# Performance work log

Hardware: AMD Instinct MI355X
Metric: run time of the kernel (lower is better)

## Reference

```python
import jax, jax.numpy as jnp
import numpy as np

B, Lq, D = 2, 4096, 768
NH, NP, NL = 6, 4, 1
Hs, Ws = 128, 128
Lf = Hs * Ws
DH = D // NH
EPS = 1e-6


def _ln(x, g, b):
    m = jnp.mean(x, -1, keepdims=True)
    v = jnp.mean(jnp.square(x - m), -1, keepdims=True)
    return (x - m) * jax.lax.rsqrt(v + EPS) * g + b


def setup_inputs() -> dict:
    key = jax.random.key(0)
    ks = jax.random.split(key, 20)
    s = 0.02
    rn = lambda k, shape, sc=s: (jax.random.normal(k, shape, jnp.float32) * sc)
    return {
        'query': jax.random.normal(ks[0], (B, Lq, D), jnp.float32),
        'reference_points': jax.random.uniform(ks[1], (B, Lq, NL, 2), jnp.float32),
        'feat': jax.random.normal(ks[2], (B, Lf, D), jnp.float32),
        'feat_other_modalities': jax.random.normal(ks[3], (B, Lq, D), jnp.float32),
        'spatial_shapes': jnp.array([[Hs, Ws]], jnp.int32),
        'level_start_index': jnp.array([0], jnp.int32),
        'qn_g': jnp.ones(D), 'qn_b': jnp.zeros(D),
        'fn_g': jnp.ones(D), 'fn_b': jnp.zeros(D),
        'W_off': rn(ks[4], (D, NH * NL * NP * 2)), 'b_off': jnp.zeros(NH * NL * NP * 2),
        'W_attn': rn(ks[5], (D, NH * NL * NP)), 'b_attn': jnp.zeros(NH * NL * NP),
        'W_val': rn(ks[6], (D, D)), 'b_val': jnp.zeros(D),
        'W_out': rn(ks[7], (D, D)), 'b_out': jnp.zeros(D),
        'gamma': rn(ks[8], (D,), 0.1),
        'qnm_g': jnp.ones(D), 'qnm_b': jnp.zeros(D),
        'fnm_g': jnp.ones(D), 'fnm_b': jnp.zeros(D),
        'ada_w0': rn(ks[9], (D, D // 4)), 'ada_b0': jnp.zeros(D // 4),
        'ada_w1': rn(ks[10], (D, D // 4)), 'ada_b1': jnp.zeros(D // 4),
        'ada_w2': rn(ks[11], (D // 4, D)), 'ada_b2': jnp.zeros(D),
        'gamma_om': rn(ks[12], (D,), 0.1),
    }


def _msdeform_attn(query_n, reference_points, feat_n, Hi, Wi,
                   W_off, b_off, W_attn, b_attn, W_val, b_val, W_out, b_out):
    Bv = query_n.shape[0]
    value = (feat_n @ W_val + b_val).reshape(Bv, Lf, NH, DH)
    value = value.transpose(0, 2, 1, 3)  # (B, NH, Lf, DH)

    off = (query_n @ W_off + b_off).reshape(Bv, Lq, NH, NL, NP, 2)
    aw = (query_n @ W_attn + b_attn).reshape(Bv, Lq, NH, NL * NP)
    aw = jax.nn.softmax(aw, axis=-1).reshape(Bv, Lq, NH, NL, NP)

    normalizer = jnp.array([Wi, Hi], jnp.float32)  # [W, H]
    loc = reference_points[:, :, None, :, None, :] + off / normalizer  # (B,Lq,NH,NL,NP,2)
    loc = loc[:, :, :, 0]  # single level -> (B, Lq, NH, NP, 2)

    # grid_sample align_corners=False, padding zeros
    x = loc[..., 0] * Wi - 0.5
    y = loc[..., 1] * Hi - 0.5
    x0 = jnp.floor(x); y0 = jnp.floor(y)
    wx1 = x - x0; wx0 = 1.0 - wx1
    wy1 = y - y0; wy0 = 1.0 - wy1
    x0i = x0.astype(jnp.int32); y0i = y0.astype(jnp.int32)
    x1i = x0i + 1; y1i = y0i + 1

    def t(a):  # (B,Lq,NH,NP) -> (B,NH,Lq,NP,1)
        return a.transpose(0, 2, 1, 3)[..., None]

    def gather(yy, xx):
        valid = (xx >= 0) & (xx < Wi) & (yy >= 0) & (yy < Hi)
        idx = jnp.clip(yy, 0, Hi - 1) * Wi + jnp.clip(xx, 0, Wi - 1)  # (B,Lq,NH,NP)
        idx = idx.transpose(0, 2, 1, 3).reshape(Bv, NH, Lq * NP)
        g = jnp.take_along_axis(value, idx[..., None], axis=2)  # (B,NH,Lq*NP,DH)
        g = g.reshape(Bv, NH, Lq, NP, DH)
        return g * t(valid.astype(jnp.float32))

    sampled = (gather(y0i, x0i) * t(wy0 * wx0) + gather(y0i, x1i) * t(wy0 * wx1)
               + gather(y1i, x0i) * t(wy1 * wx0) + gather(y1i, x1i) * t(wy1 * wx1))
    awT = aw[:, :, :, 0].transpose(0, 2, 1, 3)[..., None]  # (B,NH,Lq,NP,1)
    out = jnp.sum(sampled * awT, axis=3)  # (B,NH,Lq,DH)
    out = out.transpose(0, 2, 1, 3).reshape(Bv, Lq, D)
    return out @ W_out + b_out


def reference(query, reference_points, feat, feat_other_modalities, spatial_shapes,
              level_start_index, qn_g, qn_b, fn_g, fn_b, W_off, b_off, W_attn, b_attn,
              W_val, b_val, W_out, b_out, gamma, qnm_g, qnm_b, fnm_g, fnm_b,
              ada_w0, ada_b0, ada_w1, ada_b1, ada_w2, ada_b2, gamma_om):
    Hi = int(np.asarray(spatial_shapes)[0, 0]); Wi = int(np.asarray(spatial_shapes)[0, 1])
    query_n = _ln(query, qn_g, qn_b)
    feat_n = _ln(feat, fn_g, fn_b)
    attn = _msdeform_attn(query_n, reference_points, feat_n, Hi, Wi,
                          W_off, b_off, W_attn, b_attn, W_val, b_val, W_out, b_out)
    q = query + gamma * attn
    fom_n = _ln(feat_other_modalities, fnm_g, fnm_b)
    qn2 = _ln(q, qnm_g, qnm_b)
    p = qn2 @ ada_w0 + ada_b0
    xm = fom_n @ ada_w1 + ada_b1
    prompted = (p + xm) @ ada_w2 + ada_b2
    q = q + gamma_om * prompted
    return (q, prompted)
```

## Files before the change

### kernel.cpp

```cpp
#include <hip/hip_runtime.h>
#include <hip/hip_bf16.h>

typedef long long i64;

#define B_   2
#define LQ   4096
#define D_   768
#define NH_  6
#define NP_  4
#define DH_  128
#define LF   16384
#define NQ_ROWS (B_*LQ)
#define NF_ROWS (B_*LF)
#define QSIZE (NQ_ROWS*D_)
#define LN2_BLOCKS (2*NQ_ROWS/8)

typedef __bf16 bf16x8 __attribute__((ext_vector_type(8)));
typedef float  f32x4  __attribute__((ext_vector_type(4)));

__device__ __forceinline__ int probe_bf(const void* probe) {
  return (*(const unsigned*)probe == 0x3F803F80u) ? 1 : 0;
}
__device__ __forceinline__ float load_in(const void* p, i64 i, int bf) {
  if (bf) return __bfloat162float(((const __hip_bfloat16*)p)[i]);
  return ((const float*)p)[i];
}
__device__ __forceinline__ float us2f(unsigned short u) {
  unsigned v = (unsigned)u << 16;
  return __uint_as_float(v);
}
__device__ __forceinline__ unsigned short f2us(float f) {
  __hip_bfloat16 h = __float2bfloat16(f);
  return *(unsigned short*)&h;
}

#define NCVT 17
struct CvtArgs { const void* src[NCVT]; const void* src2[NCVT]; float* dst[NCVT]; int n[NCVT]; const void* probe; };
__global__ void k_cvt(CvtArgs a) {
  int bf = probe_bf(a.probe);
  int ai = blockIdx.y;
  int n = a.n[ai];
  const void* s = a.src[ai];
  const void* s2 = a.src2[ai];
  float* d = a.dst[ai];
  for (int i = blockIdx.x * blockDim.x + threadIdx.x; i < n; i += gridDim.x * blockDim.x) {
    float v = load_in(s, i, bf);
    if (s2) v += load_in(s2, i, bf);
    d[i] = v;
  }
}

__global__ void k_colsum(const void* w, const void* g, const void* b,
                         float* c, float* d, const void* probe) {
  __shared__ float red[2][4][64];
  int bf = probe_bf(probe);
  int l = threadIdx.x & 63;
  int kc = threadIdx.x >> 6;
  int j = blockIdx.x * 64 + l;
  int k0 = kc * 192;
  float cs = 0.f, ds = 0.f;
  #pragma unroll 8
  for (int k = 0; k < 192; ++k) {
    float wv = load_in(w, (i64)(k0 + k) * 768 + j, bf);
    cs += load_in(g, k0 + k, bf) * wv;
    ds += load_in(b, k0 + k, bf) * wv;
  }
  red[0][kc][l] = cs; red[1][kc][l] = ds;
  __syncthreads();
  if (kc == 0) {
    c[j] = red[0][0][l] + red[0][1][l] + red[0][2][l] + red[0][3][l];
    d[j] = red[1][0][l] + red[1][1][l] + red[1][2][l] + red[1][3][l];
  }
}

__device__ __forceinline__ void ln_load_bf16(const void* src, i64 so, int sl, uint4* u) {
  const unsigned short* s = (const unsigned short*)src + so;
  #pragma unroll
  for (int j = 0; j < 3; ++j) u[j] = *(const uint4*)(s + (i64)(j * 32 + sl) * 8);
}
__device__ __forceinline__ void ln_load_f32(const void* src, i64 so, int sl, float4* w) {
  const float* s = (const float*)src + so;
  #pragma unroll
  for (int j = 0; j < 3; ++j) {
    w[2*j]   = *(const float4*)(s + (i64)(j * 32 + sl) * 8);
    w[2*j+1] = *(const float4*)(s + (i64)(j * 32 + sl) * 8 + 4);
  }
}
__device__ __forceinline__ void ln_unpack_bf16(const uint4* u, float* v) {
  #pragma unroll
  for (int j = 0; j < 3; ++j) {
    uint4 t = u[j];
    v[j*8+0] = us2f((unsigned short)t.x); v[j*8+1] = us2f((unsigned short)(t.x >> 16));
    v[j*8+2] = us2f((unsigned short)t.y); v[j*8+3] = us2f((unsigned short)(t.y >> 16));
    v[j*8+4] = us2f((unsigned short)t.z); v[j*8+5] = us2f((unsigned short)(t.z >> 16));
    v[j*8+6] = us2f((unsigned short)t.w); v[j*8+7] = us2f((unsigned short)(t.w >> 16));
  }
}
__device__ __forceinline__ void ln_unpack_f32(const float4* w, float* v) {
  #pragma unroll
  for (int j = 0; j < 6; ++j) {
    v[j*4+0] = w[j].x; v[j*4+1] = w[j].y; v[j*4+2] = w[j].z; v[j*4+3] = w[j].w;
  }
}
__device__ __forceinline__ void ln_finish(const float* v, const float* g, const float* b,
                                          unsigned short* dp, int sl) {
  float s1 = 0.f, s2 = 0.f;
  #pragma unroll
  for (int i = 0; i < 24; ++i) { s1 += v[i]; s2 += v[i] * v[i]; }
  #pragma unroll
  for (int o = 16; o > 0; o >>= 1) { s1 += __shfl_xor(s1, o, 64); s2 += __shfl_xor(s2, o, 64); }
  float mean = s1 * (1.f / 768.f);
  float var  = s2 * (1.f / 768.f) - mean * mean;
  float rstd = rsqrtf(var + 1e-6f);
  #pragma unroll
  for (int j = 0; j < 3; ++j) {
    int gi = (j * 32 + sl) * 8;
    float4 g0 = *(const float4*)(g + gi), g1 = *(const float4*)(g + gi + 4);
    float4 b0 = *(const float4*)(b + gi), b1 = *(const float4*)(b + gi + 4);
    uint4 o;
    o.x = (unsigned)f2us((v[j*8+0]-mean)*rstd*g0.x+b0.x) | ((unsigned)f2us((v[j*8+1]-mean)*rstd*g0.y+b0.y) << 16);
    o.y = (unsigned)f2us((v[j*8+2]-mean)*rstd*g0.z+b0.z) | ((unsigned)f2us((v[j*8+3]-mean)*rstd*g0.w+b0.w) << 16);
    o.z = (unsigned)f2us((v[j*8+4]-mean)*rstd*g1.x+b1.x) | ((unsigned)f2us((v[j*8+5]-mean)*rstd*g1.y+b1.y) << 16);
    o.w = (unsigned)f2us((v[j*8+6]-mean)*rstd*g1.z+b1.z) | ((unsigned)f2us((v[j*8+7]-mean)*rstd*g1.w+b1.w) << 16);
    *(uint4*)(dp + gi) = o;
  }
}

#define NTT 7
struct StageArgs {
  const void* tsrc[NTT]; __hip_bfloat16* tdst[NTT];
  const void* tscale[NTT];
  int K[NTT]; int N[NTT]; int Nt[NTT]; int ds[NTT];
  int tileBase[NTT]; int tilesN[NTT];
  const void* query; const void* fom;
  const float *qg, *qb, *mg, *mb;
  __hip_bfloat16 *qn, *qnf;
  void* qraw;
  const void* probe;
};
__global__ void k_stage(StageArgs a) {
  __shared__ float lds[64][65];
  int bf = probe_bf(a.probe);
  if ((int)blockIdx.x >= LN2_BLOCKS) {
    int t = blockIdx.x - LN2_BLOCKS;
    int e = 0;
    #pragma unroll
    for (int i = 1; i < NTT; ++i) if (t >= a.tileBase[i]) e = i;
    int lt = t - a.tileBase[e];
    int tn = lt % a.tilesN[e], tk = lt / a.tilesN[e];
    int K = a.K[e], N = a.N[e], Nt = a.Nt[e], ds = a.ds[e];
    int k0 = tk * 64, n0 = tn * 64;
    int tid = threadIdx.x;
    int cl = tid & 63, rw = tid >> 6;
    const void* s = a.tsrc[e];
    const void* sc = a.tscale[e];
    #pragma unroll
    for (int i = 0; i < 16; ++i) {
      int kl = rw * 16 + i;
      int n = n0 + cl;
      float v = (n < N) ? load_in(s, (i64)(k0 + kl) * N + n, bf) : 0.f;
      if (sc) v *= load_in(sc, k0 + kl, bf);
      lds[kl][cl] = v;
    }
    __syncthreads();
    __hip_bfloat16* d = a.tdst[e];
    #pragma unroll
    for (int i = 0; i < 16; ++i) {
      int nl = rw * 16 + i;
      int n = n0 + nl;
      if (n < Nt) d[(i64)n * ds + k0 + cl] = __float2bfloat16(lds[cl][nl]);
    }
    return;
  }
  int row = blockIdx.x * 8 + (threadIdx.x >> 5);
  int sl = threadIdx.x & 31;
  const void* s; const float *g, *b; unsigned short* dp; i64 so; int kind; int lr;
  if (row < NQ_ROWS) {
    kind = 1; lr = row; s = a.query; so = (i64)lr * 768;
    g = a.qg; b = a.qb; dp = (unsigned short*)a.qn + (i64)lr * 768;
  } else {
    kind = 2; lr = row - NQ_ROWS; s = a.fom; so = (i64)lr * 768;
    g = a.mg; b = a.mb; dp = (unsigned short*)a.qnf + (i64)lr * 1536 + 768;
  }
  float v[24];
  if (bf) {
    uint4 u[3];
    ln_load_bf16(s, so, sl, u);
    if (kind == 1) {
      unsigned short* qr = (unsigned short*)a.qraw + (i64)lr * 768;
      #pragma unroll
      for (int j = 0; j < 3; ++j) *(uint4*)(qr + (i64)(j * 32 + sl) * 8) = u[j];
    }
    ln_unpack_bf16(u, v);
  } else {
    float4 w[6];
    ln_load_f32(s, so, sl, w);
    if (kind == 1) {
      float* qr = (float*)a.qraw + (i64)lr * 768;
      #pragma unroll
      for (int j = 0; j < 3; ++j) {
        *(float4*)(qr + (i64)(j * 32 + sl) * 8)     = w[2*j];
        *(float4*)(qr + (i64)(j * 32 + sl) * 8 + 4) = w[2*j+1];
      }
    }
    ln_unpack_f32(w, v);
  }
  ln_finish(v, g, b, dp, sl);
}

__global__ void k_ln_q(const float* src, const float* g, const float* b, __hip_bfloat16* dst) {
  int hw = blockIdx.x * 8 + (threadIdx.x >> 5);
  int sl = threadIdx.x & 31;
  int r = hw * 2;
  float4 w0[6], w1[6];
  ln_load_f32(src, (i64)r * 768, sl, w0);
  ln_load_f32(src, (i64)(r + 1) * 768, sl, w1);
  float v[24];
  ln_unpack_f32(w0, v);
  ln_finish(v, g, b, (unsigned short*)dst + (i64)r * 1536, sl);
  ln_unpack_f32(w1, v);
  ln_finish(v, g, b, (unsigned short*)dst + (i64)(r + 1) * 1536, sl);
}

__device__ __forceinline__ void load_lds16(const void* g, void* l) {
  __builtin_amdgcn_global_load_lds((__attribute__((address_space(1))) void*)g,
                                   (__attribute__((address_space(3))) void*)l, 16, 0, 0);
}

__global__ void k_vgemm(const void* __restrict__ Araw, const __hip_bfloat16* __restrict__ Wt,
                        const float* __restrict__ bias, __hip_bfloat16* __restrict__ Cp,
                        const float* __restrict__ cv, const float* __restrict__ dv,
                        const void* probe) {
  __shared__ __align__(16) __hip_bfloat16 sm[2 * 8192];
  __shared__ float rowstat[128][2];
  __hip_bfloat16* As = sm;
  __hip_bfloat16* Bs = sm + 8192;
  const int tid  = threadIdx.x;
  const int w    = tid >> 6, lane = tid & 63;
  const int quad = lane >> 4, l15 = lane & 15;
  const int f = blockIdx.x;
  const int xcd = f & 7, s8 = f >> 3;
  const int bn = (s8 % 6) * 128;
  const int bm = (xcd + (s8 / 6) * 8) * 128;
  const int wm = (w >> 1) * 64, wn = (w & 1) * 64;
  const int bfv = probe_bf(probe);

  {
    int sl = tid & 31, hw = tid >> 5;
    #pragma unroll 2
    for (int pass = 0; pass < 16; ++pass) {
      int r = pass * 8 + hw;
      float v[24];
      if (bfv) { uint4 u[3]; ln_load_bf16(Araw, (i64)(bm + r) * 768, sl, u); ln_unpack_bf16(u, v); }
      else     { float4 wv[6]; ln_load_f32(Araw, (i64)(bm + r) * 768, sl, wv); ln_unpack_f32(wv, v); }
      float s1 = 0.f, s2 = 0.f;
      #pragma unroll
      for (int i = 0; i < 24; ++i) { s1 += v[i]; s2 += v[i] * v[i]; }
      #pragma unroll
      for (int o = 16; o > 0; o >>= 1) { s1 += __shfl_xor(s1, o, 64); s2 += __shfl_xor(s2, o, 64); }
      if (sl == 0) {
        float mean = s1 * (1.f / 768.f);
        float var  = s2 * (1.f / 768.f) - mean * mean;
        float rstd = rsqrtf(var + 1e-6f);
        rowstat[r][0] = rstd; rowstat[r][1] = -rstd * mean;
      }
    }
  }
  __syncthreads();

  int rowS[4], colS[4];
  #pragma unroll
  for (int j = 0; j < 4; ++j) {
    int p = j * 256 + tid;
    int r = p >> 3, pc = p & 7;
    rowS[j] = r; colS[j] = (pc ^ (r & 7)) * 8;
  }

  f32x4 acc[4][4];
  #pragma unroll
  for (int i = 0; i < 4; ++i)
    #pragma unroll
    for (int j = 0; j < 4; ++j) acc[i][j] = (f32x4){0.f, 0.f, 0.f, 0.f};

  const __hip_bfloat16* Ab = (const __hip_bfloat16*)Araw + (i64)bm * 768;
  const __hip_bfloat16* Bb = Wt + (i64)bn * 768;

  for (int k0 = 0; k0 < 768; k0 += 64) {
    if (bfv) {
      #pragma unroll
      for (int j = 0; j < 4; ++j)
        load_lds16(Ab + (i64)rowS[j] * 768 + k0 + colS[j], As + (j * 256 + w * 64) * 8);
    } else {
      #pragma unroll
      for (int j = 0; j < 4; ++j) {
        int p = j * 256 + tid;
        int r = p >> 3, pc = p & 7;
        const float* src = (const float*)Araw + (i64)(bm + r) * 768 + k0 + pc * 8;
        float4 x0 = *(const float4*)src;
        float4 x1 = *(const float4*)(src + 4);
        uint4 o;
        o.x = (unsigned)f2us(x0.x) | ((unsigned)f2us(x0.y) << 16);
        o.y = (unsigned)f2us(x0.z) | ((unsigned)f2us(x0.w) << 16);
        o.z = (unsigned)f2us(x1.x) | ((unsigned)f2us(x1.y) << 16);
        o.w = (unsigned)f2us(x1.z) | ((unsigned)f2us(x1.w) << 16);
        *(uint4*)(As + ((i64)r * 8 + (pc ^ (r & 7))) * 8) = o;
      }
    }
    #pragma unroll
    for (int j = 0; j < 4; ++j)
      load_lds16(Bb + (i64)rowS[j] * 768 + k0 + colS[j], Bs + (j * 256 + w * 64) * 8);
    __syncthreads();
    bf16x8 af[2][4], bg[2][4];
    #pragma unroll
    for (int s = 0; s < 2; ++s) {
      #pragma unroll
      for (int i = 0; i < 4; ++i) {
        int ra = wm + i * 16 + l15;
        af[s][i] = *(const bf16x8*)(As + (ra * 8 + ((s * 4 + quad) ^ (ra & 7))) * 8);
        int rb = wn + i * 16 + l15;
        bg[s][i] = *(const bf16x8*)(Bs + (rb * 8 + ((s * 4 + quad) ^ (rb & 7))) * 8);
      }
    }
    #pragma unroll
    for (int s = 0; s < 2; ++s)
      #pragma unroll
      for (int i = 0; i < 4; ++i)
        #pragma unroll
        for (int j = 0; j < 4; ++j)
          acc[i][j] = __builtin_amdgcn_mfma_f32_16x16x32_bf16(af[s][i], bg[s][j], acc[i][j], 0, 0, 0);
    __syncthreads();
  }

  #pragma unroll
  for (int j = 0; j < 4; ++j) {
    int col = bn + wn + j * 16 + l15;
    float cj = cv[col], dj = dv[col] + bias[col];
    #pragma unroll
    for (int i = 0; i < 4; ++i) {
      #pragma unroll
      for (int r = 0; r < 4; ++r) {
        int lr = wm + i * 16 + quad * 4 + r;
        float v = rowstat[lr][0] * acc[i][j][r] + rowstat[lr][1] * cj + dj;
        Cp[(i64)(bm + lr) * 768 + col] = __float2bfloat16(v);
      }
    }
  }
}

template<int EPI>
__global__ void k_mgemm(const __hip_bfloat16* __restrict__ A, const __hip_bfloat16* __restrict__ Wt,
                        const float* __restrict__ bias, void* __restrict__ Cp,
                        int M, int N, int K, int Nx,
                        const void* aux0, const float* __restrict__ aux1, const void* probe) {
  __shared__ __align__(16) __hip_bfloat16 sm[2 * 8192];
  __hip_bfloat16* As = sm;
  __hip_bfloat16* Bs = sm + 8192;
  const int tid  = threadIdx.x;
  const int w    = tid >> 6, lane = tid & 63;
  const int quad = lane >> 4, l15 = lane & 15;
  const int f = blockIdx.x;
  const int xcd = f & 7, s8 = f >> 3;
  const int bn = (s8 % Nx) * 128;
  const int bm = (xcd + (s8 / Nx) * 8) * 128;
  const int wm = (w >> 1) * 64, wn = (w & 1) * 64;
  const int bfv = (EPI == 2 || EPI == 3) ? probe_bf(probe) : 0;

  int rowS[4], colS[4];
  #pragma unroll
  for (int j = 0; j < 4; ++j) {
    int p = j * 256 + tid;
    int r = p >> 3, pc = p & 7;
    rowS[j] = r; colS[j] = (pc ^ (r & 7)) * 8;
  }

  f32x4 acc[4][4];
  #pragma unroll
  for (int i = 0; i < 4; ++i)
    #pragma unroll
    for (int j = 0; j < 4; ++j) acc[i][j] = (f32x4){0.f, 0.f, 0.f, 0.f};

  const __hip_bfloat16* Ab = A  + (i64)bm * K;
  const __hip_bfloat16* Bb = Wt + (i64)bn * K;

  for (int k0 = 0; k0 < K; k0 += 64) {
    #pragma unroll
    for (int j = 0; j < 4; ++j) {
      load_lds16(Ab + (i64)rowS[j] * K + k0 + colS[j], As + (j * 256 + w * 64) * 8);
      load_lds16(Bb + (i64)rowS[j] * K + k0 + colS[j], Bs + (j * 256 + w * 64) * 8);
    }
    __syncthreads();
    bf16x8 af[2][4], bg[2][4];
    #pragma unroll
    for (int s = 0; s < 2; ++s) {
      #pragma unroll
      for (int i = 0; i < 4; ++i) {
        int ra = wm + i * 16 + l15;
        af[s][i] = *(const bf16x8*)(As + (ra * 8 + ((s * 4 + quad) ^ (ra & 7))) * 8);
        int rb = wn + i * 16 + l15;
        bg[s][i] = *(const bf16x8*)(Bs + (rb * 8 + ((s * 4 + quad) ^ (rb & 7))) * 8);
      }
    }
    #pragma unroll
    for (int s = 0; s < 2; ++s)
      #pragma unroll
      for (int i = 0; i < 4; ++i)
        #pragma unroll
        for (int j = 0; j < 4; ++j)
          acc[i][j] = __builtin_amdgcn_mfma_f32_16x16x32_bf16(af[s][i], bg[s][j], acc[i][j], 0, 0, 0);
    __syncthreads();
  }

  #pragma unroll
  for (int j = 0; j < 4; ++j) {
    int col = bn + wn + j * 16 + l15;
    if (col >= N) continue;
    float bv = bias[col];
    #pragma unroll
    for (int i = 0; i < 4; ++i) {
      #pragma unroll
      for (int r = 0; r < 4; ++r) {
        int row = bm + wm + i * 16 + quad * 4 + r;
        float v = acc[i][j][r] + bv;
        i64 idx = (i64)row * N + col;
        if (EPI == 0) {
          ((__hip_bfloat16*)Cp)[idx] = __float2bfloat16(v);
        } else if (EPI == 1) {
          ((float*)Cp)[idx] = v;
        } else if (EPI == 2) {
          ((float*)Cp)[idx] = load_in(aux0, idx, bfv) + aux1[col] * v;
        } else {
          float qv = ((const float*)aux0)[idx] + aux1[col] * v;
          if (bfv) {
            ((__hip_bfloat16*)Cp)[idx]         = __float2bfloat16(qv);
            ((__hip_bfloat16*)Cp)[QSIZE + idx] = __float2bfloat16(v);
          } else {
            ((float*)Cp)[idx]         = qv;
            ((float*)Cp)[QSIZE + idx] = v;
          }
        }
      }
    }
  }
}

__global__ void k_sample(const __hip_bfloat16* __restrict__ val, const float* __restrict__ ref,
                         const float* __restrict__ oa, const int* __restrict__ ss,
                         __hip_bfloat16* __restrict__ out) {
  int gw = blockIdx.x * 4 + (threadIdx.x >> 6);
  if (gw >= NQ_ROWS) return;
  int lane = threadIdx.x & 63;
  int sg = lane >> 4, sl = lane & 15;
  int bq = gw, b = bq >> 12;
  int Hi = ss[0], Wi = ss[1];
  float Wf = (float)Wi, Hf = (float)Hi;
  float rx = ref[(i64)bq*2], ry = ref[(i64)bq*2 + 1];
  const float* orow = oa + (i64)bq * 72;
  const __hip_bfloat16* vb = val + (i64)b * LF * D_;
  int cx = sg & 1, cy = sg >> 1;
  #pragma unroll
  for (int h = 0; h < NH_; ++h) {
    const float* ap = orow + 48 + h*4;
    float a0 = ap[0], a1 = ap[1], a2 = ap[2], a3 = ap[3];
    float mx = fmaxf(fmaxf(a0, a1), fmaxf(a2, a3));
    float e0 = __expf(a0-mx), e1 = __expf(a1-mx), e2 = __expf(a2-mx), e3 = __expf(a3-mx);
    float inv = 1.0f / (e0+e1+e2+e3);
    float wts[4] = {e0*inv, e1*inv, e2*inv, e3*inv};
    const float* op = orow + h*8;
    float acc[8];
    #pragma unroll
    for (int e = 0; e < 8; ++e) acc[e] = 0.f;
    #pragma unroll
    for (int p = 0; p < NP_; ++p) {
      float x = rx*Wf + op[p*2+0] - 0.5f;
      float y = ry*Hf + op[p*2+1] - 0.5f;
      float xf = floorf(x), yf = floorf(y);
      int x0 = (int)xf, y0 = (int)yf;
      float wx1 = x - xf, wy1 = y - yf;
      int xi = x0 + cx, yi = y0 + cy;
      float wgt = wts[p] * (cx ? wx1 : 1.f - wx1) * (cy ? wy1 : 1.f - wy1);
      if (xi >= 0 && xi < Wi && yi >= 0 && yi < Hi) {
        bf16x8 g = *(const bf16x8*)(vb + (i64)(yi*Wi + xi)*D_ + h*DH_ + sl*8);
        #pragma unroll
        for (int e = 0; e < 8; ++e) acc[e] += wgt * (float)g[e];
      }
    }
    #pragma unroll
    for (int e = 0; e < 8; ++e) {
      acc[e] += __shfl_xor(acc[e], 16, 64);
      acc[e] += __shfl_xor(acc[e], 32, 64);
    }
    if (sg == 0) {
      uint4 o;
      o.x = (unsigned)f2us(acc[0]) | ((unsigned)f2us(acc[1]) << 16);
      o.y = (unsigned)f2us(acc[2]) | ((unsigned)f2us(acc[3]) << 16);
      o.z = (unsigned)f2us(acc[4]) | ((unsigned)f2us(acc[5]) << 16);
      o.w = (unsigned)f2us(acc[6]) | ((unsigned)f2us(acc[7]) << 16);
      *(uint4*)(out + (i64)bq*D_ + h*DH_ + sl*8) = o;
    }
  }
}

extern "C" void kernel_launch(void* const* d_in, const int* in_sizes, int n_in,
                              void* d_out, int out_size, void* d_ws, size_t ws_size,
                              hipStream_t stream) {
  char* base = (char*)d_ws;
  size_t o = 0;
  auto alloc = [&](size_t bytes) { size_t r = o; o += (bytes + 63) & ~(size_t)63; return r; };
  auto F = [&](size_t off) { return (float*)(base + off); };
  auto H = [&](size_t off) { return (__hip_bfloat16*)(base + off); };
  const void* probe = d_in[6];

  size_t REF   = alloc(NQ_ROWS*2*4);
  size_t QN_G  = alloc(768*4); size_t QN_B = alloc(768*4);
  size_t FN_G  = alloc(768*4); size_t FN_B = alloc(768*4);
  size_t BOA   = alloc(128*4);
  size_t BVAL  = alloc(768*4); size_t BOUT = alloc(768*4);
  size_t GAMMA = alloc(768*4);
  size_t QNM_G = alloc(768*4); size_t QNM_B = alloc(768*4);
  size_t FNM_G = alloc(768*4); size_t FNM_B = alloc(768*4);
  size_t AB01  = alloc(192*4);
  size_t AB2   = alloc(768*4); size_t GOM  = alloc(768*4);
  size_t CV    = alloc(768*4); size_t DV   = alloc(768*4);
  size_t WT_VAL = alloc((size_t)768*768*2);
  size_t WT_OUT = alloc((size_t)768*768*2);
  size_t WT_OA  = alloc((size_t)128*768*2);
  size_t WT_A01 = alloc((size_t)256*1536*2);
  size_t WT_A2  = alloc((size_t)768*192*2);
  size_t VALUE  = alloc((size_t)NF_ROWS*768*2);
  size_t QN     = alloc((size_t)NQ_ROWS*768*2);
  size_t QRAW   = alloc((size_t)QSIZE*4);
  size_t QNF    = alloc((size_t)NQ_ROWS*1536*2);
  size_t ATTNP  = alloc((size_t)NQ_ROWS*768*2);
  size_t PXM    = alloc((size_t)NQ_ROWS*192*2);
  size_t OA     = alloc((size_t)NQ_ROWS*72*4);
  size_t QBUF   = alloc((size_t)QSIZE*4);

  {
    CvtArgs ca;
    const int   idx[NCVT]  = {1,6,7,8,9,11,13,15,17,18,19,20,21,22,24,28,29};
    const size_t dof[NCVT] = {REF,QN_G,QN_B,FN_G,FN_B,BOA,BOA+48*4,BVAL,BOUT,GAMMA,
                              QNM_G,QNM_B,FNM_G,FNM_B,AB01,AB2,GOM};
    for (int i = 0; i < NCVT; ++i) {
      ca.src[i] = d_in[idx[i]]; ca.src2[i] = nullptr;
      ca.dst[i] = F(dof[i]); ca.n[i] = in_sizes[idx[i]];
    }
    ca.src2[14] = d_in[26];
    ca.probe = probe;
    k_cvt<<<dim3(8, NCVT), 256, 0, stream>>>(ca);
  }
  k_colsum<<<12, 256, 0, stream>>>(d_in[14], d_in[8], d_in[9], F(CV), F(DV), probe);

  int tb = 0;
  {
    StageArgs sa;
    const int   src[NTT]  = {14, 16, 10, 12, 23, 25, 27};
    const size_t dst[NTT] = {WT_VAL, WT_OUT, WT_OA, WT_OA + (size_t)48*768*2,
                             WT_A01, WT_A01 + (size_t)768*2, WT_A2};
    const int Kk[NTT] = {768, 768, 768, 768, 768,  768, 192};
    const int Nn[NTT] = {768, 768,  48,  24, 192,  192, 768};
    const int Nt[NTT] = {768, 768,  48,  80, 256,  256, 768};
    const int Ds[NTT] = {768, 768, 768, 768, 1536, 1536, 192};
    const void* sc[NTT] = {d_in[8], nullptr, nullptr, nullptr, nullptr, nullptr, nullptr};
    for (int i = 0; i < NTT; ++i) {
      sa.tsrc[i] = d_in[src[i]]; sa.tdst[i] = H(dst[i]); sa.tscale[i] = sc[i];
      sa.K[i] = Kk[i]; sa.N[i] = Nn[i]; sa.Nt[i] = Nt[i]; sa.ds[i] = Ds[i];
      sa.tilesN[i] = (Nt[i] + 63) / 64;
      sa.tileBase[i] = tb;
      tb += sa.tilesN[i] * (Kk[i] / 64);
    }
    sa.query = d_in[0]; sa.fom = d_in[3];
    sa.qg = F(QN_G);  sa.qb = F(QN_B);
    sa.mg = F(FNM_G); sa.mb = F(FNM_B);
    sa.qn = H(QN); sa.qnf = H(QNF);
    sa.qraw = base + QRAW;
    sa.probe = probe;
    k_stage<<<LN2_BLOCKS + tb, 256, 0, stream>>>(sa);
  }

  k_vgemm<<<256*6, 256, 0, stream>>>(d_in[2], H(WT_VAL), F(BVAL), H(VALUE),
                                     F(CV), F(DV), probe);
  k_mgemm<1><<<64*1, 256, 0, stream>>>(H(QN), H(WT_OA), F(BOA), F(OA),
                                       NQ_ROWS, 72, 768, 1, nullptr, nullptr, probe);
  k_sample<<<NQ_ROWS/4, 256, 0, stream>>>(H(VALUE), F(REF), F(OA), (const int*)d_in[4], H(ATTNP));
  k_mgemm<2><<<64*6, 256, 0, stream>>>(H(ATTNP), H(WT_OUT), F(BOUT), F(QBUF),
                                       NQ_ROWS, 768, 768, 6, base + QRAW, F(GAMMA), probe);
  k_ln_q<<<NQ_ROWS/16, 256, 0, stream>>>(F(QBUF), F(QNM_G), F(QNM_B), H(QNF));
  k_mgemm<0><<<64*2, 256, 0, stream>>>(H(QNF), H(WT_A01), F(AB01), H(PXM),
                                       NQ_ROWS, 192, 1536, 2, nullptr, nullptr, probe);
  k_mgemm<3><<<64*6, 256, 0, stream>>>(H(PXM), H(WT_A2), F(AB2), d_out,
                                       NQ_ROWS, 768, 192, 6, F(QBUF), F(GOM), probe);
}
```

Measured before the change: 565.6 us.

## Compute feature LayerNorm stats inside value GEMM loop and fold colsum into stage kernel

The value GEMM no longer runs a separate prologue pass over its 128-row A tile to compute LayerNorm mean and rstd. Instead it accumulates the sums and squared sums from the A tiles it already loads each K step, then reduces them with shuffles before the epilogue. The bf16 path now uses register loads and LDS stores instead of direct-to-LDS loads, which adds register pressure. The separate k_colsum launch is folded into k_stage as 12 extra blocks, removing one kernel launch.

```diff
diff --git a/kernel.cpp b/kernel.cpp
--- a/kernel.cpp
+++ b/kernel.cpp
@@ -50,29 +50,6 @@
   }
 }
 
-__global__ void k_colsum(const void* w, const void* g, const void* b,
-                         float* c, float* d, const void* probe) {
-  __shared__ float red[2][4][64];
-  int bf = probe_bf(probe);
-  int l = threadIdx.x & 63;
-  int kc = threadIdx.x >> 6;
-  int j = blockIdx.x * 64 + l;
-  int k0 = kc * 192;
-  float cs = 0.f, ds = 0.f;
-  #pragma unroll 8
-  for (int k = 0; k < 192; ++k) {
-    float wv = load_in(w, (i64)(k0 + k) * 768 + j, bf);
-    cs += load_in(g, k0 + k, bf) * wv;
-    ds += load_in(b, k0 + k, bf) * wv;
-  }
-  red[0][kc][l] = cs; red[1][kc][l] = ds;
-  __syncthreads();
-  if (kc == 0) {
-    c[j] = red[0][0][l] + red[0][1][l] + red[0][2][l] + red[0][3][l];
-    d[j] = red[1][0][l] + red[1][1][l] + red[1][2][l] + red[1][3][l];
-  }
-}
-
 __device__ __forceinline__ void ln_load_bf16(const void* src, i64 so, int sl, uint4* u) {
   const unsigned short* s = (const unsigned short*)src + so;
   #pragma unroll
@@ -132,6 +109,9 @@
   const void* tscale[NTT];
   int K[NTT]; int N[NTT]; int Nt[NTT]; int ds[NTT];
   int tileBase[NTT]; int tilesN[NTT];
+  int csBase;
+  const void* csw; const void* csg; const void* csb;
+  float* csc; float* csd;
   const void* query; const void* fom;
   const float *qg, *qb, *mg, *mb;
   __hip_bfloat16 *qn, *qnf;
@@ -143,6 +123,28 @@
   int bf = probe_bf(a.probe);
   if ((int)blockIdx.x >= LN2_BLOCKS) {
     int t = blockIdx.x - LN2_BLOCKS;
+    if (t >= a.csBase) {
+      float (*red)[4][64] = (float(*)[4][64])lds;
+      int lb = t - a.csBase;
+      int l = threadIdx.x & 63;
+      int kc = threadIdx.x >> 6;
+      int j = lb * 64 + l;
+      int k0 = kc * 192;
+      float cs = 0.f, ds = 0.f;
+      #pragma unroll 8
+      for (int k = 0; k < 192; ++k) {
+        float wv = load_in(a.csw, (i64)(k0 + k) * 768 + j, bf);
+        cs += load_in(a.csg, k0 + k, bf) * wv;
+        ds += load_in(a.csb, k0 + k, bf) * wv;
+      }
+      red[0][kc][l] = cs; red[1][kc][l] = ds;
+      __syncthreads();
+      if (kc == 0) {
+        a.csc[j] = red[0][0][l] + red[0][1][l] + red[0][2][l] + red[0][3][l];
+        a.csd[j] = red[1][0][l] + red[1][1][l] + red[1][2][l] + red[1][3][l];
+      }
+      return;
+    }
     int e = 0;
     #pragma unroll
     for (int i = 1; i < NTT; ++i) if (t >= a.tileBase[i]) e = i;
@@ -245,29 +247,6 @@
   const int wm = (w >> 1) * 64, wn = (w & 1) * 64;
   const int bfv = probe_bf(probe);
 
-  {
-    int sl = tid & 31, hw = tid >> 5;
-    #pragma unroll 2
-    for (int pass = 0; pass < 16; ++pass) {
-      int r = pass * 8 + hw;
-      float v[24];
-      if (bfv) { uint4 u[3]; ln_load_bf16(Araw, (i64)(bm + r) * 768, sl, u); ln_unpack_bf16(u, v); }
-      else     { float4 wv[6]; ln_load_f32(Araw, (i64)(bm + r) * 768, sl, wv); ln_unpack_f32(wv, v); }
-      float s1 = 0.f, s2 = 0.f;
-      #pragma unroll
-      for (int i = 0; i < 24; ++i) { s1 += v[i]; s2 += v[i] * v[i]; }
-      #pragma unroll
-      for (int o = 16; o > 0; o >>= 1) { s1 += __shfl_xor(s1, o, 64); s2 += __shfl_xor(s2, o, 64); }
-      if (sl == 0) {
-        float mean = s1 * (1.f / 768.f);
-        float var  = s2 * (1.f / 768.f) - mean * mean;
-        float rstd = rsqrtf(var + 1e-6f);
-        rowstat[r][0] = rstd; rowstat[r][1] = -rstd * mean;
-      }
-    }
-  }
-  __syncthreads();
-
   int rowS[4], colS[4];
   #pragma unroll
   for (int j = 0; j < 4; ++j) {
@@ -281,15 +260,32 @@
   for (int i = 0; i < 4; ++i)
     #pragma unroll
     for (int j = 0; j < 4; ++j) acc[i][j] = (f32x4){0.f, 0.f, 0.f, 0.f};
+  float st1[4] = {0.f, 0.f, 0.f, 0.f};
+  float st2[4] = {0.f, 0.f, 0.f, 0.f};
 
   const __hip_bfloat16* Ab = (const __hip_bfloat16*)Araw + (i64)bm * 768;
   const __hip_bfloat16* Bb = Wt + (i64)bn * 768;
 
   for (int k0 = 0; k0 < 768; k0 += 64) {
+    #pragma unroll
+    for (int j = 0; j < 4; ++j)
+      load_lds16(Bb + (i64)rowS[j] * 768 + k0 + colS[j], Bs + (j * 256 + w * 64) * 8);
     if (bfv) {
       #pragma unroll
-      for (int j = 0; j < 4; ++j)
-        load_lds16(Ab + (i64)rowS[j] * 768 + k0 + colS[j], As + (j * 256 + w * 64) * 8);
+      for (int j = 0; j < 4; ++j) {
+        int p = j * 256 + tid;
+        int r = p >> 3, pc = p & 7;
+        const unsigned short* src = (const unsigned short*)Araw + (i64)(bm + r) * 768 + k0 + pc * 8;
+        uint4 u = *(const uint4*)src;
+        float v0 = us2f((unsigned short)u.x), v1 = us2f((unsigned short)(u.x >> 16));
+        float v2 = us2f((unsigned short)u.y), v3 = us2f((unsigned short)(u.y >> 16));
+        float v4 = us2f((unsigned short)u.z), v5 = us2f((unsigned short)(u.z >> 16));
+        float v6 = us2f((unsigned short)u.w), v7 = us2f((unsigned short)(u.w >> 16));
+        st1[j] += ((v0 + v1) + (v2 + v3)) + ((v4 + v5) + (v6 + v7));
+        st2[j] = fmaf(v0, v0, fmaf(v1, v1, fmaf(v2, v2, fmaf(v3, v3,
+                 fmaf(v4, v4, fmaf(v5, v5, fmaf(v6, v6, fmaf(v7, v7, st2[j]))))))));
+        *(uint4*)(As + ((i64)r * 8 + (pc ^ (r & 7))) * 8) = u;
+      }
     } else {
       #pragma unroll
       for (int j = 0; j < 4; ++j) {
@@ -298,6 +294,9 @@
         const float* src = (const float*)Araw + (i64)(bm + r) * 768 + k0 + pc * 8;
         float4 x0 = *(const float4*)src;
         float4 x1 = *(const float4*)(src + 4);
+        st1[j] += ((x0.x + x0.y) + (x0.z + x0.w)) + ((x1.x + x1.y) + (x1.z + x1.w));
+        st2[j] = fmaf(x0.x, x0.x, fmaf(x0.y, x0.y, fmaf(x0.z, x0.z, fmaf(x0.w, x0.w,
+                 fmaf(x1.x, x1.x, fmaf(x1.y, x1.y, fmaf(x1.z, x1.z, fmaf(x1.w, x1.w, st2[j]))))))));
         uint4 o;
         o.x = (unsigned)f2us(x0.x) | ((unsigned)f2us(x0.y) << 16);
         o.y = (unsigned)f2us(x0.z) | ((unsigned)f2us(x0.w) << 16);
@@ -306,30 +305,45 @@
         *(uint4*)(As + ((i64)r * 8 + (pc ^ (r & 7))) * 8) = o;
       }
     }
-    #pragma unroll
-    for (int j = 0; j < 4; ++j)
-      load_lds16(Bb + (i64)rowS[j] * 768 + k0 + colS[j], Bs + (j * 256 + w * 64) * 8);
     __syncthreads();
-    bf16x8 af[2][4], bg[2][4];
-    #pragma unroll
-    for (int s = 0; s < 2; ++s) {
-      #pragma unroll
-      for (int i = 0; i < 4; ++i) {
-        int ra = wm + i * 16 + l15;
-        af[s][i] = *(const bf16x8*)(As + (ra * 8 + ((s * 4 + quad) ^ (ra & 7))) * 8);
-        int rb = wn + i * 16 + l15;
-        bg[s][i] = *(const bf16x8*)(Bs + (rb * 8 + ((s * 4 + quad) ^ (rb & 7))) * 8);
-      }
-    }
-    #pragma unroll
-    for (int s = 0; s < 2; ++s)
-      #pragma unroll
-      for (int i = 0; i < 4; ++i)
+    {
+      bf16x8 af[2][4], bg[2][4];
+      #pragma unroll
+      for (int s = 0; s < 2; ++s) {
         #pragma unroll
-        for (int j = 0; j < 4; ++j)
-          acc[i][j] = __builtin_amdgcn_mfma_f32_16x16x32_bf16(af[s][i], bg[s][j], acc[i][j], 0, 0, 0);
+        for (int i = 0; i < 4; ++i) {
+          int ra = wm + i * 16 + l15;
+          af[s][i] = *(const bf16x8*)(As + (ra * 8 + ((s * 4 + quad) ^ (ra & 7))) * 8);
+          int rb = wn + i * 16 + l15;
+          bg[s][i] = *(const bf16x8*)(Bs + (rb * 8 + ((s * 4 + quad) ^ (rb & 7))) * 8);
+        }
+      }
+      #pragma unroll
+      for (int s = 0; s < 2; ++s)
+        #pragma unroll
+        for (int i = 0; i < 4; ++i)
+          #pragma unroll
+          for (int j = 0; j < 4; ++j)
+            acc[i][j] = __builtin_amdgcn_mfma_f32_16x16x32_bf16(af[s][i], bg[s][j], acc[i][j], 0, 0, 0);
+    }
     __syncthreads();
   }
+
+  #pragma unroll
+  for (int j = 0; j < 4; ++j) {
+    float s1 = st1[j], s2 = st2[j];
+    s1 += __shfl_xor(s1, 1, 64); s2 += __shfl_xor(s2, 1, 64);
+    s1 += __shfl_xor(s1, 2, 64); s2 += __shfl_xor(s2, 2, 64);
+    s1 += __shfl_xor(s1, 4, 64); s2 += __shfl_xor(s2, 4, 64);
+    if ((tid & 7) == 0) {
+      int r = rowS[j];
+      float mean = s1 * (1.f / 768.f);
+      float var  = s2 * (1.f / 768.f) - mean * mean;
+      float rstd = rsqrtf(var + 1e-6f);
+      rowstat[r][0] = rstd; rowstat[r][1] = -rstd * mean;
+    }
+  }
+  __syncthreads();
 
   #pragma unroll
   for (int j = 0; j < 4; ++j) {
@@ -548,7 +562,6 @@
     ca.probe = probe;
     k_cvt<<<dim3(8, NCVT), 256, 0, stream>>>(ca);
   }
-  k_colsum<<<12, 256, 0, stream>>>(d_in[14], d_in[8], d_in[9], F(CV), F(DV), probe);
 
   int tb = 0;
   {
@@ -568,13 +581,16 @@
       sa.tileBase[i] = tb;
       tb += sa.tilesN[i] * (Kk[i] / 64);
     }
+    sa.csBase = tb;
+    sa.csw = d_in[14]; sa.csg = d_in[8]; sa.csb = d_in[9];
+    sa.csc = F(CV); sa.csd = F(DV);
     sa.query = d_in[0]; sa.fom = d_in[3];
     sa.qg = F(QN_G);  sa.qb = F(QN_B);
     sa.mg = F(FNM_G); sa.mb = F(FNM_B);
     sa.qn = H(QN); sa.qnf = H(QNF);
     sa.qraw = base + QRAW;
     sa.probe = probe;
-    k_stage<<<LN2_BLOCKS + tb, 256, 0, stream>>>(sa);
+    k_stage<<<LN2_BLOCKS + tb + 12, 256, 0, stream>>>(sa);
   }
 
   k_vgemm<<<256*6, 256, 0, stream>>>(d_in[2], H(WT_VAL), F(BVAL), H(VALUE),
```

After: 594.8 us. 1.05x slower.
